# Kernel tuning notes

Measured on AMD Instinct MI355X. Metric: run time of the kernel, lower is better.

Reference implementation:

```python
import jax, jax.numpy as jnp
import numpy as np

DIN = 1024
DIM = 1024
NUM_HEADS = 16
HEAD_DIM = DIM // NUM_HEADS
SEQ_LEN = 2048
BATCH = 2


def setup_inputs() -> dict:
    key = jax.random.key(0)
    ks = jax.random.split(key, 5)
    s = 0.02
    x = jax.random.normal(ks[0], (BATCH, SEQ_LEN, DIN), dtype=jnp.float32)
    # torch nn.Linear weights are (out_features, in_features)
    wq = jax.random.normal(ks[1], (DIM, DIN), dtype=jnp.float32) * s
    wk = jax.random.normal(ks[2], (DIM, DIN), dtype=jnp.float32) * s
    wv = jax.random.normal(ks[3], (DIM, DIN), dtype=jnp.float32) * s
    wo = jax.random.normal(ks[4], (DIM, DIM), dtype=jnp.float32) * s
    return {"x": x, "wq": wq, "wk": wk, "wv": wv, "wo": wo}


def reference(x, wq, wk, wv, wo):
    bs, seq_len, _ = x.shape
    # project and split heads: [b, h, s, d]
    def split(z):
        return z.reshape(bs, seq_len, NUM_HEADS, HEAD_DIM).transpose(0, 2, 1, 3)
    q = split(x @ wq.T)
    k = split(x @ wk.T)
    v = split(x @ wv.T)
    # raw scores, causal mask applied BEFORE the 1/sqrt(d) scaling (as in source;
    # -inf is invariant to positive scaling so math matches standard causal attn)
    att = jnp.einsum('bhqd,bhkd->bhqk', q, k)
    causal = jnp.triu(jnp.ones((seq_len, seq_len), dtype=bool), k=1)
    att = jnp.where(causal, -jnp.inf, att)
    att = jax.nn.softmax(att / jnp.sqrt(jnp.float32(HEAD_DIM)), axis=-1)
    ctx = jnp.einsum('bhqk,bhkd->bhqd', att, v)
    ctx = ctx.transpose(0, 2, 1, 3).reshape(bs, seq_len, DIM)
    return ctx @ wo.T
```

## Files before the change

### kernel.cpp

```cpp
#include <hip/hip_runtime.h>
#include <stdint.h>

#define DIN 1024
#define DIMM 1024
#define NH 16
#define HD 64
#define SEQ 2048
#define BATCH 2
#define MTOT (BATCH*SEQ)
#define SCALE 0.125f

typedef __bf16 bf16;
typedef __bf16 bf16x8 __attribute__((ext_vector_type(8)));
typedef __bf16 bf16x4 __attribute__((ext_vector_type(4)));
typedef float f32x4 __attribute__((ext_vector_type(4)));

__device__ __forceinline__ void async16(bf16* lds, const bf16* g) {
  __builtin_amdgcn_global_load_lds(
      (const __attribute__((address_space(1))) void*)g,
      (__attribute__((address_space(3))) void*)lds, 16, 0, 0);
}

__global__ __launch_bounds__(256) void convert_all(const float* __restrict__ x,
                                                   const float* __restrict__ wq,
                                                   const float* __restrict__ wk,
                                                   const float* __restrict__ wv,
                                                   const float* __restrict__ wo,
                                                   bf16* __restrict__ xb,
                                                   bf16* __restrict__ Wb) {
  const int t = blockIdx.x * 256 + threadIdx.x;
#pragma unroll
  for (int i = 0; i < 4; ++i) {
    const int c = t + i * 262144;
    const float* src;
    bf16* dst;
    if (c < 524288) {
      src = x + (size_t)c * 8;
      dst = xb + (size_t)c * 8;
    } else {
      const int cw = c - 524288;
      const int w = cw >> 17;
      const int off = (cw & 131071) * 8;
      const float* wp = (w == 0) ? wq : (w == 1) ? wk : (w == 2) ? wv : wo;
      src = wp + off;
      dst = Wb + (size_t)w * 1048576 + off;
    }
    f32x4 a = *(const f32x4*)src;
    f32x4 b = *(const f32x4*)(src + 4);
    bf16x8 r;
    r[0] = (bf16)a[0]; r[1] = (bf16)a[1]; r[2] = (bf16)a[2]; r[3] = (bf16)a[3];
    r[4] = (bf16)b[0]; r[5] = (bf16)b[1]; r[6] = (bf16)b[2]; r[7] = (bf16)b[3];
    *(bf16x8*)dst = r;
  }
}

__global__ __launch_bounds__(512, 2) void qkv_gemm(const bf16* __restrict__ A,
                                                   const bf16* __restrict__ B,
                                                   bf16* __restrict__ Q,
                                                   bf16* __restrict__ Kb,
                                                   bf16* __restrict__ Vt) {
  __shared__ bf16 As0[256 * 64];
  __shared__ bf16 Bs0[192 * 64];
  __shared__ bf16 As1[256 * 64];
  __shared__ bf16 Bs1[192 * 64];
  const int tid  = threadIdx.x;
  const int lane = tid & 63;
  const int wave = tid >> 6;
  const int lrow = lane & 15;
  const int quad = lane >> 4;
  const int wrow = wave >> 1;
  const int wcol = wave & 1;
  const int lin  = blockIdx.x;
  const int xcd  = lin & 7;
  const int idx  = lin >> 3;
  const int nbase = (xcd * 2 + (idx & 1)) * 192;
  const int mbase = (idx >> 1) * 256;

  const int srow = tid >> 3;
  const int sdst = srow * 64 + (tid & 7) * 8;
  const int sx   = ((tid & 7) ^ (srow & 7)) * 8;

  const bf16* ap = A + (size_t)(mbase + srow) * DIN + sx;
  const bf16* bp = B + (size_t)(nbase + srow) * DIN + sx;

  f32x4 acc[4][6] = {};

#define QKV_STAGE(Asb, Bsb)                                          \
  do {                                                               \
    _Pragma("unroll")                                                \
    for (int i = 0; i < 4; ++i)                                      \
      async16(&Asb[sdst + i * 4096], ap + (size_t)i * 64 * DIN);     \
    _Pragma("unroll")                                                \
    for (int i = 0; i < 3; ++i)                                      \
      async16(&Bsb[sdst + i * 4096], bp + (size_t)i * 64 * DIN);     \
  } while (0)

#define QKV_COMPUTE(Asb, Bsb)                                        \
  do {                                                               \
    __builtin_amdgcn_s_setprio(1);                                   \
    _Pragma("unroll")                                                \
    for (int h = 0; h < 2; ++h) {                                    \
      const int cx = ((h * 4 + quad) ^ (lrow & 7)) * 8;              \
      bf16x8 af[4], bfr[6];                                          \
      _Pragma("unroll")                                              \
      for (int i = 0; i < 4; ++i)                                    \
        af[i] = *(const bf16x8*)&Asb[(wrow * 64 + i * 16 + lrow) * 64 + cx]; \
      _Pragma("unroll")                                              \
      for (int j = 0; j < 6; ++j)                                    \
        bfr[j] = *(const bf16x8*)&Bsb[(wcol * 96 + j * 16 + lrow) * 64 + cx]; \
      _Pragma("unroll")                                              \
      for (int i = 0; i < 4; ++i)                                    \
        _Pragma("unroll")                                            \
        for (int j = 0; j < 6; ++j)                                  \
          acc[i][j] = __builtin_amdgcn_mfma_f32_16x16x32_bf16(af[i], bfr[j], acc[i][j], 0, 0, 0); \
    }                                                                \
    __builtin_amdgcn_s_setprio(0);                                   \
  } while (0)

#define WAIT_VM(n)  asm volatile("s_waitcnt vmcnt(" #n ")" ::: "memory")
#define BARRIER()   asm volatile("s_barrier" ::: "memory")

  QKV_STAGE(As0, Bs0);
  WAIT_VM(0);
  BARRIER();

#pragma unroll 1
  for (int t = 0; t < 16; t += 2) {
    if (t + 1 < 16) {
      ap += 64; bp += 64;
      QKV_STAGE(As1, Bs1);
      WAIT_VM(7);
    } else {
      WAIT_VM(0);
    }
    BARRIER();
    QKV_COMPUTE(As0, Bs0);
    BARRIER();
    if (t + 1 < 16) {
      if (t + 2 < 16) {
        ap += 64; bp += 64;
        QKV_STAGE(As0, Bs0);
        WAIT_VM(7);
      } else {
        WAIT_VM(0);
      }
      BARRIER();
      QKV_COMPUTE(As1, Bs1);
      BARRIER();
    }
  }

#undef QKV_STAGE
#undef QKV_COMPUTE
#undef WAIT_VM
#undef BARRIER

#pragma unroll
  for (int mt = 0; mt < 4; ++mt) {
    const int m0 = mbase + wrow * 64 + mt * 16 + quad * 4;
#pragma unroll
    for (int nt = 0; nt < 6; ++nt) {
      const int n16 = nbase + wcol * 96 + nt * 16;
      const int n = n16 + lrow;
      if (n16 < 1024) {
#pragma unroll
        for (int rr = 0; rr < 4; ++rr)
          Q[(size_t)(m0 + rr) * 1024 + n] = (bf16)acc[mt][nt][rr];
      } else if (n16 < 2048) {
#pragma unroll
        for (int rr = 0; rr < 4; ++rr)
          Kb[(size_t)(m0 + rr) * 1024 + (n - 1024)] = (bf16)acc[mt][nt][rr];
      } else {
        const int nn = n - 2048;
        const int row = ((m0 >> 11) * 16 + (nn >> 6)) * 64 + (nn & 63);
        bf16x4 ov;
#pragma unroll
        for (int rr = 0; rr < 4; ++rr) ov[rr] = (bf16)acc[mt][nt][rr];
        *(bf16x4*)&Vt[(size_t)row * SEQ + (m0 & 2047)] = ov;
      }
    }
  }
}

__global__ __launch_bounds__(256) void proj_gemm(const bf16* __restrict__ A,
                                                 const bf16* __restrict__ B,
                                                 float* __restrict__ C) {
  __shared__ bf16 As[128 * 64];
  __shared__ bf16 Bs[64 * 64];
  const int tid  = threadIdx.x;
  const int lane = tid & 63;
  const int wave = tid >> 6;
  const int lrow = lane & 15;
  const int quad = lane >> 4;
  const int wr = (wave >> 1) * 64;
  const int wc = (wave & 1) * 32;
  const int lin = blockIdx.x;
  const int xcd = lin & 7;
  const int idx = lin >> 3;
  const int nbase = (xcd * 2 + (idx & 1)) * 64;
  const int mbase = (idx >> 1) * 128;
  const int srow = tid >> 3;
  const int scol = (tid & 7) * 8;
  const int sx   = ((tid & 7) ^ (srow & 7)) * 8;

  f32x4 acc[4][2] = {};

  for (int k0 = 0; k0 < DIMM; k0 += 64) {
#pragma unroll
    for (int i = 0; i < 4; ++i)
      async16(&As[(i * 32 + srow) * 64 + scol],
              &A[(size_t)(mbase + i * 32 + srow) * DIMM + k0 + sx]);
#pragma unroll
    for (int i = 0; i < 2; ++i)
      async16(&Bs[(i * 32 + srow) * 64 + scol],
              &B[(size_t)(nbase + i * 32 + srow) * DIMM + k0 + sx]);
    __syncthreads();
#pragma unroll
    for (int h = 0; h < 2; ++h) {
      const int cx = ((h * 4 + quad) ^ (lrow & 7)) * 8;
      bf16x8 af[4], bfr[2];
#pragma unroll
      for (int i = 0; i < 4; ++i)
        af[i] = *(const bf16x8*)&As[(wr + i * 16 + lrow) * 64 + cx];
#pragma unroll
      for (int i = 0; i < 2; ++i)
        bfr[i] = *(const bf16x8*)&Bs[(wc + i * 16 + lrow) * 64 + cx];
#pragma unroll
      for (int mt = 0; mt < 4; ++mt)
#pragma unroll
        for (int nt = 0; nt < 2; ++nt)
          acc[mt][nt] = __builtin_amdgcn_mfma_f32_16x16x32_bf16(af[mt], bfr[nt], acc[mt][nt], 0, 0, 0);
    }
    __syncthreads();
  }

#pragma unroll
  for (int mt = 0; mt < 4; ++mt) {
    const int m0 = mbase + wr + mt * 16 + quad * 4;
#pragma unroll
    for (int nt = 0; nt < 2; ++nt) {
      const int n = nbase + wc + nt * 16 + lrow;
#pragma unroll
      for (int rr = 0; rr < 4; ++rr)
        C[(size_t)(m0 + rr) * 1024 + n] = acc[mt][nt][rr];
    }
  }
}

__global__ __launch_bounds__(256, 5) void attn(const bf16* __restrict__ Q,
                                               const bf16* __restrict__ K,
                                               const bf16* __restrict__ Vt,
                                               bf16* __restrict__ O) {
  __shared__ bf16 Ks[2][64 * 64];
  __shared__ bf16 Vts[2][64 * 64];
  const int tid  = threadIdx.x;
  const int wave = tid >> 6;
  const int lane = tid & 63;
  const int lrow = lane & 15;
  const int quad = lane >> 4;
  const int lin  = blockIdx.x;
  const int bh   = lin & 31;
  const int j    = lin >> 5;
  const int t    = j & 7;
  const int grp  = j >> 3;
  const int qi   = (grp == 0) ? (31 - t) : (grp == 1) ? t
                 : (grp == 2) ? (23 - t) : (8 + t);
  const int b = bh >> 4;
  const int h = bh & 15;
  const int qw = qi * 64 + wave * 16;
  const int ntiles = qi + 1;

  const bf16* Qh  = Q  + (size_t)(b * SEQ) * DIMM + h * HD;
  const bf16* Kh  = K  + (size_t)(b * SEQ) * DIMM + h * HD;
  const bf16* Vth = Vt + (size_t)bh * 64 * SEQ;

  const int srow = tid >> 3;
  const int sdst = srow * 64 + (tid & 7) * 8;
  const int sx   = ((tid & 7) ^ (srow & 7)) * 8;
  const int cx0 = ((0 + quad) ^ (lrow & 7)) * 8;
  const int cx1 = ((4 + quad) ^ (lrow & 7)) * 8;
  const int LL = lrow & 7;
  const int qh = quad >> 1, ql = quad & 1;
  int vc[4];
#pragma unroll
  for (int g = 0; g < 4; ++g)
    vc[g] = ((((2 * g + qh) ^ LL) << 1) | ql) * 4;

  bf16x8 qf0 = *(const bf16x8*)&Qh[(size_t)(qw + lrow) * DIMM + quad * 8];
  bf16x8 qf1 = *(const bf16x8*)&Qh[(size_t)(qw + lrow) * DIMM + 32 + quad * 8];

  const bf16* kg0 = Kh + (size_t)srow * DIMM + sx;
  const bf16* kg1 = kg0 + (size_t)32 * DIMM;
  const bf16* vg0 = Vth + (size_t)srow * SEQ + sx;
  const bf16* vg1 = vg0 + (size_t)32 * SEQ;

  async16(&Ks[0][sdst],         kg0);
  async16(&Ks[0][sdst + 2048],  kg1);
  async16(&Vts[0][sdst],        vg0);
  async16(&Vts[0][sdst + 2048], vg1);
  __syncthreads();

  float lsum = 0.f;
  f32x4 o_acc[4] = {};
  int cur = 0;
  const float C1 = 0.18033688f;

  for (int kt = 0; kt < ntiles; ++kt) {
    if (kt + 1 < ntiles) {
      kg0 += 64 * DIMM; kg1 += 64 * DIMM; vg0 += 64; vg1 += 64;
      bf16* Kn = Ks[cur ^ 1];
      bf16* Vn = Vts[cur ^ 1];
      async16(&Kn[sdst],        kg0);
      async16(&Kn[sdst + 2048], kg1);
      async16(&Vn[sdst],        vg0);
      async16(&Vn[sdst + 2048], vg1);
    }
    const bf16* Kc = Ks[cur];
    const bf16* Vc = Vts[cur];
    f32x4 s[4] = {};
#pragma unroll
    for (int gg = 0; gg < 4; ++gg) {
      bf16x8 kf0 = *(const bf16x8*)&Kc[(gg * 16 + lrow) * 64 + cx0];
      bf16x8 kf1 = *(const bf16x8*)&Kc[(gg * 16 + lrow) * 64 + cx1];
      s[gg] = __builtin_amdgcn_mfma_f32_16x16x32_bf16(kf0, qf0, s[gg], 0, 0, 0);
      s[gg] = __builtin_amdgcn_mfma_f32_16x16x32_bf16(kf1, qf1, s[gg], 0, 0, 0);
    }
    if (kt == qi) {
      const int qrow = qw + lrow;
      const int kbase = kt * 64;
#pragma unroll
      for (int gg = 0; gg < 4; ++gg)
#pragma unroll
        for (int r = 0; r < 4; ++r)
          s[gg][r] = (kbase + gg * 16 + quad * 4 + r > qrow) ? -1e30f : s[gg][r];
    }
    bf16x8 pf0, pf1;
#pragma unroll
    for (int gg = 0; gg < 4; ++gg)
#pragma unroll
      for (int r = 0; r < 4; ++r) {
        const float p = __builtin_amdgcn_exp2f(s[gg][r] * C1);
        lsum += p;
        if (gg < 2) pf0[(gg & 1) * 4 + r] = (bf16)p;
        else        pf1[(gg & 1) * 4 + r] = (bf16)p;
      }
#pragma unroll
    for (int dt = 0; dt < 4; ++dt) {
      const bf16* Vr = &Vc[(dt * 16 + lrow) * 64];
      bf16x4 a0 = *(const bf16x4*)&Vr[vc[0]];
      bf16x4 a1 = *(const bf16x4*)&Vr[vc[1]];
      bf16x4 b0 = *(const bf16x4*)&Vr[vc[2]];
      bf16x4 b1 = *(const bf16x4*)&Vr[vc[3]];
      bf16x8 vfA = __builtin_shufflevector(a0, a1, 0, 1, 2, 3, 4, 5, 6, 7);
      bf16x8 vfB = __builtin_shufflevector(b0, b1, 0, 1, 2, 3, 4, 5, 6, 7);
      o_acc[dt] = __builtin_amdgcn_mfma_f32_16x16x32_bf16(vfA, pf0, o_acc[dt], 0, 0, 0);
      o_acc[dt] = __builtin_amdgcn_mfma_f32_16x16x32_bf16(vfB, pf1, o_acc[dt], 0, 0, 0);
    }
    __syncthreads();
    cur ^= 1;
  }

  lsum += __shfl_xor(lsum, 16);
  lsum += __shfl_xor(lsum, 32);
  const float rl = __builtin_amdgcn_rcpf(lsum);
  bf16* Ob = O + (size_t)(b * SEQ + qw + lrow) * DIMM + h * HD;
#pragma unroll
  for (int dt = 0; dt < 4; ++dt) {
    bf16x4 ov;
#pragma unroll
    for (int r = 0; r < 4; ++r)
      ov[r] = (bf16)(o_acc[dt][r] * rl);
    *(bf16x4*)&Ob[dt * 16 + quad * 4] = ov;
  }
}

extern "C" void kernel_launch(void* const* d_in, const int* in_sizes, int n_in,
                              void* d_out, int out_size, void* d_ws, size_t ws_size,
                              hipStream_t stream) {
  const float* x  = (const float*)d_in[0];
  const float* wq = (const float*)d_in[1];
  const float* wk = (const float*)d_in[2];
  const float* wv = (const float*)d_in[3];
  const float* wo = (const float*)d_in[4];

  const size_t M4 = (size_t)MTOT * DIMM;
  bf16* xb  = (bf16*)d_ws;
  bf16* Wb  = xb + M4;
  bf16* Q   = Wb + M4;
  bf16* Kb  = Q + M4;
  bf16* Vt  = Kb + M4;
  bf16* CTX = xb;
  float* out = (float*)d_out;

  convert_all<<<dim3(1024), dim3(256), 0, stream>>>(x, wq, wk, wv, wo, xb, Wb);
  qkv_gemm<<<dim3(256), dim3(512), 0, stream>>>(xb, Wb, Q, Kb, Vt);
  attn<<<dim3(BATCH * NH * (SEQ / 64)), dim3(256), 0, stream>>>(Q, Kb, Vt, CTX);
  proj_gemm<<<dim3(512), dim3(256), 0, stream>>>(CTX, Wb + 3 * 1048576, out);
}
```

Measured before the change: 169.8 us.

## Shrink QKV GEMM tile to 128x192 and double-buffer projection GEMM

The QKV GEMM moves from 512-thread blocks with 256x192 tiles to 256-thread blocks with 128x192 tiles, doubling the grid to 512 blocks. The staging loads and vmcnt waits are adjusted to match. The output projection GEMM gains double-buffered LDS, async prefetch of the next K-slice during compute, and raised wave priority around its MFMA loops. The goal is better load balance across CUs and overlap of global loads with compute, at the cost of lower per-block data reuse in the QKV GEMM and more LDS per projection block.

New measurement: 165.5 us. 2.5% less time.

```diff
diff --git a/kernel.cpp b/kernel.cpp
--- a/kernel.cpp
+++ b/kernel.cpp
@@ -20,6 +20,9 @@
       (const __attribute__((address_space(1))) void*)g,
       (__attribute__((address_space(3))) void*)lds, 16, 0, 0);
 }
+
+#define WAIT_VM(n)  asm volatile("s_waitcnt vmcnt(" #n ")" ::: "memory")
+#define BARRIER()   asm volatile("s_barrier" ::: "memory")
 
 __global__ __launch_bounds__(256) void convert_all(const float* __restrict__ x,
                                                    const float* __restrict__ wq,
@@ -54,14 +57,14 @@
   }
 }
 
-__global__ __launch_bounds__(512, 2) void qkv_gemm(const bf16* __restrict__ A,
+__global__ __launch_bounds__(256, 2) void qkv_gemm(const bf16* __restrict__ A,
                                                    const bf16* __restrict__ B,
                                                    bf16* __restrict__ Q,
                                                    bf16* __restrict__ Kb,
                                                    bf16* __restrict__ Vt) {
-  __shared__ bf16 As0[256 * 64];
+  __shared__ bf16 As0[128 * 64];
+  __shared__ bf16 As1[128 * 64];
   __shared__ bf16 Bs0[192 * 64];
-  __shared__ bf16 As1[256 * 64];
   __shared__ bf16 Bs1[192 * 64];
   const int tid  = threadIdx.x;
   const int lane = tid & 63;
@@ -74,7 +77,7 @@
   const int xcd  = lin & 7;
   const int idx  = lin >> 3;
   const int nbase = (xcd * 2 + (idx & 1)) * 192;
-  const int mbase = (idx >> 1) * 256;
+  const int mbase = (idx >> 1) * 128;
 
   const int srow = tid >> 3;
   const int sdst = srow * 64 + (tid & 7) * 8;
@@ -89,10 +92,10 @@
   do {                                                               \
     _Pragma("unroll")                                                \
     for (int i = 0; i < 4; ++i)                                      \
-      async16(&Asb[sdst + i * 4096], ap + (size_t)i * 64 * DIN);     \
-    _Pragma("unroll")                                                \
-    for (int i = 0; i < 3; ++i)                                      \
-      async16(&Bsb[sdst + i * 4096], bp + (size_t)i * 64 * DIN);     \
+      async16(&Asb[sdst + i * 2048], ap + (size_t)i * 32 * DIN);     \
+    _Pragma("unroll")                                                \
+    for (int i = 0; i < 6; ++i)                                      \
+      async16(&Bsb[sdst + i * 2048], bp + (size_t)i * 32 * DIN);     \
   } while (0)
 
 #define QKV_COMPUTE(Asb, Bsb)                                        \
@@ -117,43 +120,32 @@
     __builtin_amdgcn_s_setprio(0);                                   \
   } while (0)
 
-#define WAIT_VM(n)  asm volatile("s_waitcnt vmcnt(" #n ")" ::: "memory")
-#define BARRIER()   asm volatile("s_barrier" ::: "memory")
-
   QKV_STAGE(As0, Bs0);
   WAIT_VM(0);
   BARRIER();
 
 #pragma unroll 1
   for (int t = 0; t < 16; t += 2) {
-    if (t + 1 < 16) {
+    ap += 64; bp += 64;
+    QKV_STAGE(As1, Bs1);
+    WAIT_VM(10);
+    BARRIER();
+    QKV_COMPUTE(As0, Bs0);
+    BARRIER();
+    if (t + 2 < 16) {
       ap += 64; bp += 64;
-      QKV_STAGE(As1, Bs1);
-      WAIT_VM(7);
+      QKV_STAGE(As0, Bs0);
+      WAIT_VM(10);
     } else {
       WAIT_VM(0);
     }
     BARRIER();
-    QKV_COMPUTE(As0, Bs0);
-    BARRIER();
-    if (t + 1 < 16) {
-      if (t + 2 < 16) {
-        ap += 64; bp += 64;
-        QKV_STAGE(As0, Bs0);
-        WAIT_VM(7);
-      } else {
-        WAIT_VM(0);
-      }
-      BARRIER();
-      QKV_COMPUTE(As1, Bs1);
-      BARRIER();
-    }
+    QKV_COMPUTE(As1, Bs1);
+    BARRIER();
   }
 
 #undef QKV_STAGE
 #undef QKV_COMPUTE
-#undef WAIT_VM
-#undef BARRIER
 
 #pragma unroll
   for (int mt = 0; mt < 4; ++mt) {
@@ -182,11 +174,13 @@
   }
 }
 
-__global__ __launch_bounds__(256) void proj_gemm(const bf16* __restrict__ A,
-                                                 const bf16* __restrict__ B,
-                                                 float* __restrict__ C) {
-  __shared__ bf16 As[128 * 64];
-  __shared__ bf16 Bs[64 * 64];
+__global__ __launch_bounds__(256, 2) void proj_gemm(const bf16* __restrict__ A,
+                                                    const bf16* __restrict__ B,
+                                                    float* __restrict__ C) {
+  __shared__ bf16 As0[128 * 64];
+  __shared__ bf16 As1[128 * 64];
+  __shared__ bf16 Bs0[64 * 64];
+  __shared__ bf16 Bs1[64 * 64];
   const int tid  = threadIdx.x;
   const int lane = tid & 63;
   const int wave = tid >> 6;
@@ -200,39 +194,72 @@
   const int nbase = (xcd * 2 + (idx & 1)) * 64;
   const int mbase = (idx >> 1) * 128;
   const int srow = tid >> 3;
-  const int scol = (tid & 7) * 8;
+  const int sdst = srow * 64 + (tid & 7) * 8;
   const int sx   = ((tid & 7) ^ (srow & 7)) * 8;
 
+  const bf16* ap = A + (size_t)(mbase + srow) * DIMM + sx;
+  const bf16* bp = B + (size_t)(nbase + srow) * DIMM + sx;
+
   f32x4 acc[4][2] = {};
 
-  for (int k0 = 0; k0 < DIMM; k0 += 64) {
-#pragma unroll
-    for (int i = 0; i < 4; ++i)
-      async16(&As[(i * 32 + srow) * 64 + scol],
-              &A[(size_t)(mbase + i * 32 + srow) * DIMM + k0 + sx]);
-#pragma unroll
-    for (int i = 0; i < 2; ++i)
-      async16(&Bs[(i * 32 + srow) * 64 + scol],
-              &B[(size_t)(nbase + i * 32 + srow) * DIMM + k0 + sx]);
-    __syncthreads();
-#pragma unroll
-    for (int h = 0; h < 2; ++h) {
-      const int cx = ((h * 4 + quad) ^ (lrow & 7)) * 8;
-      bf16x8 af[4], bfr[2];
-#pragma unroll
-      for (int i = 0; i < 4; ++i)
-        af[i] = *(const bf16x8*)&As[(wr + i * 16 + lrow) * 64 + cx];
-#pragma unroll
-      for (int i = 0; i < 2; ++i)
-        bfr[i] = *(const bf16x8*)&Bs[(wc + i * 16 + lrow) * 64 + cx];
-#pragma unroll
-      for (int mt = 0; mt < 4; ++mt)
-#pragma unroll
-        for (int nt = 0; nt < 2; ++nt)
-          acc[mt][nt] = __builtin_amdgcn_mfma_f32_16x16x32_bf16(af[mt], bfr[nt], acc[mt][nt], 0, 0, 0);
-    }
-    __syncthreads();
-  }
+#define PRJ_STAGE(Asb, Bsb)                                          \
+  do {                                                               \
+    _Pragma("unroll")                                                \
+    for (int i = 0; i < 4; ++i)                                      \
+      async16(&Asb[sdst + i * 2048], ap + (size_t)i * 32 * DIMM);    \
+    _Pragma("unroll")                                                \
+    for (int i = 0; i < 2; ++i)                                      \
+      async16(&Bsb[sdst + i * 2048], bp + (size_t)i * 32 * DIMM);    \
+  } while (0)
+
+#define PRJ_COMPUTE(Asb, Bsb)                                        \
+  do {                                                               \
+    __builtin_amdgcn_s_setprio(1);                                   \
+    _Pragma("unroll")                                                \
+    for (int h = 0; h < 2; ++h) {                                    \
+      const int cx = ((h * 4 + quad) ^ (lrow & 7)) * 8;              \
+      bf16x8 af[4], bfr[2];                                          \
+      _Pragma("unroll")                                              \
+      for (int i = 0; i < 4; ++i)                                    \
+        af[i] = *(const bf16x8*)&Asb[(wr + i * 16 + lrow) * 64 + cx]; \
+      _Pragma("unroll")                                              \
+      for (int i = 0; i < 2; ++i)                                    \
+        bfr[i] = *(const bf16x8*)&Bsb[(wc + i * 16 + lrow) * 64 + cx]; \
+      _Pragma("unroll")                                              \
+      for (int mt = 0; mt < 4; ++mt)                                 \
+        _Pragma("unroll")                                            \
+        for (int nt = 0; nt < 2; ++nt)                               \
+          acc[mt][nt] = __builtin_amdgcn_mfma_f32_16x16x32_bf16(af[mt], bfr[nt], acc[mt][nt], 0, 0, 0); \
+    }                                                                \
+    __builtin_amdgcn_s_setprio(0);                                   \
+  } while (0)
+
+  PRJ_STAGE(As0, Bs0);
+  WAIT_VM(0);
+  BARRIER();
+
+#pragma unroll 1
+  for (int t = 0; t < 16; t += 2) {
+    ap += 64; bp += 64;
+    PRJ_STAGE(As1, Bs1);
+    WAIT_VM(6);
+    BARRIER();
+    PRJ_COMPUTE(As0, Bs0);
+    BARRIER();
+    if (t + 2 < 16) {
+      ap += 64; bp += 64;
+      PRJ_STAGE(As0, Bs0);
+      WAIT_VM(6);
+    } else {
+      WAIT_VM(0);
+    }
+    BARRIER();
+    PRJ_COMPUTE(As1, Bs1);
+    BARRIER();
+  }
+
+#undef PRJ_STAGE
+#undef PRJ_COMPUTE
 
 #pragma unroll
   for (int mt = 0; mt < 4; ++mt) {
@@ -393,7 +420,7 @@
   float* out = (float*)d_out;
 
   convert_all<<<dim3(1024), dim3(256), 0, stream>>>(x, wq, wk, wv, wo, xb, Wb);
-  qkv_gemm<<<dim3(256), dim3(512), 0, stream>>>(xb, Wb, Q, Kb, Vt);
+  qkv_gemm<<<dim3(512), dim3(256), 0, stream>>>(xb, Wb, Q, Kb, Vt);
   attn<<<dim3(BATCH * NH * (SEQ / 64)), dim3(256), 0, stream>>>(Q, Kb, Vt, CTX);
   proj_gemm<<<dim3(512), dim3(256), 0, stream>>>(CTX, Wb + 3 * 1048576, out);
 }
```
